# Kernel tuning notes

Measured on AMD Instinct MI355X. Metric: run time of the kernel, lower is better.

## Reference

```python
import jax, jax.numpy as jnp
import numpy as np

N, M = 30000, 16
NODE_F = 128          # node_fea_len
ORIG_F = 19           # 4 + location_num(15)
EDGE_F = 5
PI_IN = NODE_F + 10 + 5 + 5  # 148
BN_EPS = 1e-5


def _linear_init(k, fin, fout):
    s = 1.0 / np.sqrt(fin)
    kw, kb = jax.random.split(k)
    W = jax.random.uniform(kw, (fin, fout), jnp.float32, -s, s)
    b = jax.random.uniform(kb, (fout,), jnp.float32, -s, s)
    return W, b


def setup_inputs() -> dict:
    key = jax.random.key(0)
    ks = jax.random.split(key, 24)
    node_fea = jax.random.normal(ks[0], (N, ORIG_F), jnp.float32)
    edge_fea = jax.random.uniform(ks[1], (N, M, EDGE_F), dtype=jnp.float32)
    idx = jax.random.randint(ks[2], (N, M), 0, N)
    neg = jax.random.uniform(ks[3], (N, M)) < 0.1
    edge_fea_idx = jnp.where(neg, -1, idx)
    distance = jax.random.uniform(ks[4], (N, M), dtype=jnp.float32)

    emb_W, emb_b = _linear_init(ks[5], ORIG_F, NODE_F)
    fcW, fcB = [], []
    for i in range(3):
        W, b = _linear_init(ks[6 + i], 2 * NODE_F + EDGE_F, 2 * NODE_F)
        fcW.append(W); fcB.append(b)
    conv_fc_W = jnp.stack(fcW)   # [3, 261, 256]
    conv_fc_b = jnp.stack(fcB)   # [3, 256]
    bn1_g = jnp.ones((3, 2 * NODE_F), jnp.float32)
    bn1_b = jnp.zeros((3, 2 * NODE_F), jnp.float32)
    bn2_g = jnp.ones((3, NODE_F), jnp.float32)
    bn2_b = jnp.zeros((3, NODE_F), jnp.float32)

    def u(k, shape):  # MLP init: uniform(-0.08, 0.08)
        return jax.random.uniform(k, shape, jnp.float32, -0.08, 0.08)
    pi_W1 = u(ks[9], (PI_IN, 128)); pi_b1 = u(ks[10], (128,))
    pi_W2 = u(ks[11], (128, 256)); pi_b2 = u(ks[12], (256,))
    pi_W3 = u(ks[13], (256, 128)); pi_b3 = u(ks[14], (128,))
    pi_W4 = u(ks[15], (128, 1)); pi_b4 = u(ks[16], (1,))

    return dict(node_fea=node_fea, edge_fea=edge_fea, edge_fea_idx=edge_fea_idx,
                distance=distance, tp_type=1,
                emb_W=emb_W, emb_b=emb_b,
                conv_fc_W=conv_fc_W, conv_fc_b=conv_fc_b,
                bn1_g=bn1_g, bn1_b=bn1_b, bn2_g=bn2_g, bn2_b=bn2_b,
                pi_W1=pi_W1, pi_b1=pi_b1, pi_W2=pi_W2, pi_b2=pi_b2,
                pi_W3=pi_W3, pi_b3=pi_b3, pi_W4=pi_W4, pi_b4=pi_b4)


def _bn(x, g, b):  # BatchNorm1d in training mode: batch stats (biased var)
    mu = x.mean(0)
    var = x.var(0)
    return (x - mu) * jax.lax.rsqrt(var + BN_EPS) * g + b


def reference(node_fea, edge_fea, edge_fea_idx, distance, tp_type,
              emb_W, emb_b, conv_fc_W, conv_fc_b,
              bn1_g, bn1_b, bn2_g, bn2_b,
              pi_W1, pi_b1, pi_W2, pi_b2, pi_W3, pi_b3, pi_W4, pi_b4):
    n, m = edge_fea_idx.shape
    node = node_fea @ emb_W + emb_b                     # [N, 128]
    mask = (edge_fea_idx >= 0).astype(node.dtype)       # [N, M]

    for l in range(3):  # three CGCNN conv layers (structurally distinct params)
        nbr = node[edge_fea_idx]                        # gather, neg idx wraps like torch
        self_f = jnp.broadcast_to(node[:, None, :], (n, m, NODE_F))
        total = jnp.concatenate([self_f, nbr, edge_fea], axis=2)   # [N, M, 261]
        gated = total @ conv_fc_W[l] + conv_fc_b[l]                # [N, M, 256]
        gated = _bn(gated.reshape(-1, 2 * NODE_F), bn1_g[l], bn1_b[l]).reshape(n, m, 2 * NODE_F)
        filt, _ = jnp.split(gated, 2, axis=2)
        # NOTE: original code overwrites nbr_core with nbr_filter*mask (bug kept faithfully)
        filt = jax.nn.sigmoid(filt) * mask[..., None]
        core = filt * mask[..., None]
        summed = jnp.sum(filt * core, axis=1)                      # [N, 128]
        summed = _bn(summed, bn2_g[l], bn2_b[l])
        node = jax.nn.softplus(node + summed)

    # calculate_pi
    av = node[edge_fea_idx]                                        # [N, M, 128]
    tp_f = jnp.full((n, m, 5), float(tp_type), node.dtype)
    feat = jnp.concatenate([av,
                            jnp.tile(edge_fea, (1, 1, 2)),          # 10
                            jnp.repeat(distance[..., None], 5, 2),  # 5
                            tp_f], axis=2)                          # [N, M, 148]
    h = jax.nn.relu(feat @ pi_W1 + pi_b1)
    h = jax.nn.relu(h @ pi_W2 + pi_b2)
    h = jax.nn.relu(h @ pi_W3 + pi_b3)
    logits = h @ pi_W4 + pi_b4                                      # [N, M, 1]

    # get_action masked softmax: mask=1 where invalid
    amask = jnp.where((edge_fea_idx >= 0) & (edge_fea[:, :, 4] <= tp_type), 0.0, 1.0)
    logits_masked = logits - 1e8 * amask[..., None]
    prob = jax.nn.softmax(logits_masked.reshape(-1))                # [N*M]
    return prob
```

## Files before the change

### kernel.cpp

```cpp
#include <hip/hip_runtime.h>
#include <hip/hip_bf16.h>
#include <math.h>

#define NN 30000
#define MM 16
#define F 128
#define NMROWS (NN*MM)
constexpr float BN_EPS = 1e-5f;

using bf16x8 = __attribute__((ext_vector_type(8))) short;
using f32x4v = __attribute__((ext_vector_type(4))) float;

#define WS_NODE   0u
#define WS_S      3840000u
#define WS_T      7680000u
#define WS_SUM    11520000u
#define WS_LOGIT  15360000u
#define WS_RED    15840000u
#define WS_STATS  15841024u
#define ST_BN1SUM 0u
#define ST_BN1SQ  384u
#define ST_BN2SUM 768u
#define ST_BN2SQ  1152u
#define ST_W1E    2048u
#define ST_W1D    2688u
#define ST_B1EFF  2816u
#define ST_END    2944u

__device__ __forceinline__ float read_tp(const int* tp) {
  int ti = tp[0];
  return (ti >= -1000 && ti <= 1000) ? (float)ti : __int_as_float(ti);
}

__device__ __forceinline__ void split3(float x, short& a, short& b, short& c) {
  unsigned u0 = __float_as_uint(x);
  a = (short)(u0 >> 16);
  float r1 = x - __uint_as_float(u0 & 0xFFFF0000u);
  unsigned u1 = __float_as_uint(r1);
  b = (short)(u1 >> 16);
  float r2 = r1 - __uint_as_float(u1 & 0xFFFF0000u);
  c = (short)(__float_as_uint(r2) >> 16);
}

__global__ void k_pack_conv(const float* __restrict__ cW, const float* __restrict__ pW1,
                            short* __restrict__ convPack, short* __restrict__ wUp) {
  int tid = threadIdx.x, l = blockIdx.x;
  if (l < 3) {
    const float* Wl = cW + (size_t)l*261*256;
    short* dst = convPack + (size_t)l*98304;
    for (int it = 0; it < 8; ++it) {
      int slot = it*512 + tid;
      int ln = slot & 63, f = slot >> 6;
      int nt = f & 15, ks = f >> 4;
      int colg = nt*16 + (ln & 15);
      int kb = ks*32 + (ln >> 4)*8;
      bf16x8 h, m, lo;
      #pragma unroll
      for (int i = 0; i < 8; ++i) {
        int k = kb + i;
        float v = (colg < 128) ? Wl[(size_t)k*256 + colg]
                               : Wl[(size_t)(128 + k)*256 + (colg - 128)];
        short a, b, c; split3(v, a, b, c);
        h[i] = a; m[i] = b; lo[i] = c;
      }
      *(bf16x8*)&dst[((size_t)((0*4 + ks)*16 + nt))*512 + ln*8] = h;
      *(bf16x8*)&dst[((size_t)((1*4 + ks)*16 + nt))*512 + ln*8] = m;
      *(bf16x8*)&dst[((size_t)((2*4 + ks)*16 + nt))*512 + ln*8] = lo;
    }
  } else {
    for (int it = 0; it < 4; ++it) {
      int slot = it*512 + tid;
      int ln = slot & 63, f = slot >> 6;
      int nt = f & 7, ks = f >> 3;
      int colg = nt*16 + (ln & 15);
      int kb = ks*32 + (ln >> 4)*8;
      bf16x8 h, m, lo;
      #pragma unroll
      for (int i = 0; i < 8; ++i) {
        float v = pW1[(size_t)(kb + i)*128 + colg];
        short a, b, c; split3(v, a, b, c);
        h[i] = a; m[i] = b; lo[i] = c;
      }
      *(bf16x8*)&wUp[((size_t)((0*4 + ks)*8 + nt))*512 + ln*8] = h;
      *(bf16x8*)&wUp[((size_t)((1*4 + ks)*8 + nt))*512 + ln*8] = m;
      *(bf16x8*)&wUp[((size_t)((2*4 + ks)*8 + nt))*512 + ln*8] = lo;
    }
  }
}

__global__ __launch_bounds__(512, 2) void k_gemm(
    const float* __restrict__ nf, const float* __restrict__ embW, const float* __restrict__ embB,
    float* __restrict__ node, const float* __restrict__ summed,
    const float* __restrict__ bsum2, const float* __restrict__ bsq2,
    const float* __restrict__ g2, const float* __restrict__ b2,
    const short* __restrict__ Wp, const float* __restrict__ bias,
    float* __restrict__ outS, float* __restrict__ outT,
    int NT, int mode, int writeNode) {
  __shared__ __align__(16) short sb[64*392];
  __shared__ float nfL[64][20];
  __shared__ float ewL[19][128];
  int tid = threadIdx.x;
  int n0 = blockIdx.x*64;
  if (mode == 0) {
    for (int i = tid; i < 64*19; i += 512) {
      int r = i/19, k = i - r*19;
      int n = n0 + r;
      nfL[r][k] = (n < NN) ? nf[(size_t)n*19 + k] : 0.f;
    }
    for (int i = tid; i < 19*128; i += 512) ewL[i >> 7][i & 127] = embW[i];
  }
  __syncthreads();
  {
    int c = tid & 127, rg = tid >> 7;
    float scv = 0.f, shv = 0.f, eb = 0.f;
    if (mode == 0) {
      eb = embB[c];
    } else {
      const float inv_n = 1.f / (float)NN;
      float mu = bsum2[c]*inv_n;
      float var = bsq2[c]*inv_n - mu*mu;
      scv = g2[c]*rsqrtf(var + BN_EPS);
      shv = b2[c] - mu*scv;
    }
    #pragma unroll 4
    for (int rr = 0; rr < 16; ++rr) {
      int r = rg*16 + rr;
      int n = n0 + r;
      float v = 0.f;
      if (n < NN) {
        if (mode == 0) {
          v = eb;
          #pragma unroll
          for (int k = 0; k < 19; ++k) v = fmaf(nfL[r][k], ewL[k][c], v);
        } else {
          float x = node[(size_t)n*F + c] + fmaf(summed[(size_t)n*F + c], scv, shv);
          v = fmaxf(x, 0.f) + log1pf(expf(-fabsf(x)));
        }
        if (writeNode) node[(size_t)n*F + c] = v;
      }
      short s0, s1, s2; split3(v, s0, s1, s2);
      sb[r*392 + c] = s0; sb[r*392 + 128 + c] = s1; sb[r*392 + 256 + c] = s2;
    }
  }
  __syncthreads();
  int wv = tid >> 6, ln = tid & 63, lr = ln & 15, lg2 = ln >> 4;
  int ntpw = NT >> 3;
  f32x4v z4 = {0.f,0.f,0.f,0.f};
  f32x4v acc0[4] = {z4,z4,z4,z4};
  f32x4v acc1[4] = {z4,z4,z4,z4};
  int nt0 = wv*ntpw, nt1 = wv*ntpw + 1;
  for (int ks = 0; ks < 4; ++ks) {
    #pragma unroll
    for (int bs = 0; bs < 3; ++bs) {
      bf16x8 B0 = *(const bf16x8*)&Wp[((size_t)((bs*4 + ks)*NT + nt0))*512 + ln*8];
      bf16x8 B1 = B0;
      if (ntpw == 2) B1 = *(const bf16x8*)&Wp[((size_t)((bs*4 + ks)*NT + nt1))*512 + ln*8];
      int na = 3 - bs;
      #pragma unroll
      for (int as = 0; as < 3; ++as) {
        if (as >= na) break;
        #pragma unroll
        for (int mt = 0; mt < 4; ++mt) {
          bf16x8 a = *(const bf16x8*)&sb[(mt*16 + lr)*392 + as*128 + ks*32 + lg2*8];
          acc0[mt] = __builtin_amdgcn_mfma_f32_16x16x32_bf16(a, B0, acc0[mt], 0, 0, 0);
          if (ntpw == 2)
            acc1[mt] = __builtin_amdgcn_mfma_f32_16x16x32_bf16(a, B1, acc1[mt], 0, 0, 0);
        }
      }
    }
  }
  {
    int col = nt0*16 + lr;
    float bb = (col < 128) ? bias[col] : 0.f;
    #pragma unroll
    for (int mt = 0; mt < 4; ++mt) {
      #pragma unroll
      for (int rr = 0; rr < 4; ++rr) {
        int row = n0 + mt*16 + lg2*4 + rr;
        if (row < NN) {
          float x = acc0[mt][rr] + bb;
          if (col < 128) outS[(size_t)row*F + col] = x;
          else outT[(size_t)row*F + col - 128] = x;
        }
      }
    }
  }
  if (ntpw == 2) {
    int col = nt1*16 + lr;
    float bb = (col < 128) ? bias[col] : 0.f;
    #pragma unroll
    for (int mt = 0; mt < 4; ++mt) {
      #pragma unroll
      for (int rr = 0; rr < 4; ++rr) {
        int row = n0 + mt*16 + lg2*4 + rr;
        if (row < NN) {
          float x = acc1[mt][rr] + bb;
          if (col < 128) outS[(size_t)row*F + col] = x;
          else outT[(size_t)row*F + col - 128] = x;
        }
      }
    }
  }
}

__global__ __launch_bounds__(256, 8) void k_stats(
    const float* __restrict__ S, const float* __restrict__ T,
    const float* __restrict__ Wl, const float* __restrict__ edge,
    const int* __restrict__ idx,
    float* __restrict__ bsum, float* __restrict__ bsq) {
  __shared__ float eL[1280];
  __shared__ int gL[256];
  __shared__ float rA[256], rB[256];
  int tid = threadIdx.x;
  int n0 = blockIdx.x*16;
  for (int i = tid; i < 1280; i += 256) eL[i] = edge[(size_t)n0*80 + i];
  {
    int v = idx[n0*MM + tid];
    gL[tid] = v < 0 ? v + NN : v;
  }
  __syncthreads();
  int c = tid & 127, h = tid >> 7;
  float we[5];
  #pragma unroll
  for (int j = 0; j < 5; ++j) we[j] = Wl[(size_t)(256+j)*256 + c];
  float s1 = 0.f, s2 = 0.f;
  for (int nl = h*8; nl < h*8 + 8; ++nl) {
    float sv = S[(size_t)(n0+nl)*F + c];
    #pragma unroll
    for (int m = 0; m < MM; ++m) {
      int row = nl*MM + m;
      float g = sv + T[(size_t)gL[row]*F + c];
      const float* e = &eL[row*5];
      #pragma unroll
      for (int j = 0; j < 5; ++j) g = fmaf(e[j], we[j], g);
      s1 += g; s2 = fmaf(g, g, s2);
    }
  }
  rA[tid] = s1; rB[tid] = s2;
  __syncthreads();
  if (h == 0) {
    atomicAdd(&bsum[c], s1 + rA[128 + c]);
    atomicAdd(&bsq[c],  s2 + rB[128 + c]);
  }
}

__global__ __launch_bounds__(256, 6) void k_pass2(
    const float* __restrict__ S, const float* __restrict__ T,
    const float* __restrict__ Wl, const float* __restrict__ edge,
    const int* __restrict__ idx,
    const float* __restrict__ bsum1, const float* __restrict__ bsq1,
    const float* __restrict__ g1, const float* __restrict__ b1,
    float* __restrict__ summed, float* __restrict__ bsum2, float* __restrict__ bsq2) {
  __shared__ float eL[1280];
  __shared__ int gL[256];
  __shared__ float mk[256];
  __shared__ float rA[256], rB[256];
  int tid = threadIdx.x;
  int n0 = blockIdx.x*16;
  for (int i = tid; i < 1280; i += 256) eL[i] = edge[(size_t)n0*80 + i];
  {
    int v = idx[n0*MM + tid];
    mk[tid] = v >= 0 ? 1.f : 0.f;
    gL[tid] = v < 0 ? v + NN : v;
  }
  __syncthreads();
  int c = tid & 127, h = tid >> 7;
  float we[5];
  #pragma unroll
  for (int j = 0; j < 5; ++j) we[j] = Wl[(size_t)(256+j)*256 + c];
  float sc1v, sh1v;
  {
    const float inv_n = 1.f / (float)NMROWS;
    float mu = bsum1[c]*inv_n;
    float var = bsq1[c]*inv_n - mu*mu;
    sc1v = g1[c]*rsqrtf(var + BN_EPS);
    sh1v = b1[c] - mu*sc1v;
  }
  float st1 = 0.f, st2 = 0.f;
  for (int nl = h*8; nl < h*8 + 8; ++nl) {
    float sv = S[(size_t)(n0+nl)*F + c];
    float acc = 0.f;
    #pragma unroll
    for (int m = 0; m < MM; ++m) {
      int row = nl*MM + m;
      float g = sv + T[(size_t)gL[row]*F + c];
      const float* e = &eL[row*5];
      #pragma unroll
      for (int j = 0; j < 5; ++j) g = fmaf(e[j], we[j], g);
      float x = fmaf(g, sc1v, sh1v);
      float sig = 1.f/(1.f + expf(-x));
      acc = fmaf(mk[row]*sig, sig, acc);
    }
    summed[(size_t)(n0+nl)*F + c] = acc;
    st1 += acc; st2 = fmaf(acc, acc, st2);
  }
  rA[tid] = st1; rB[tid] = st2;
  __syncthreads();
  if (h == 0) {
    atomicAdd(&bsum2[c], st1 + rA[128 + c]);
    atomicAdd(&bsq2[c],  st2 + rB[128 + c]);
  }
}

__global__ void k_pi_const(const float* __restrict__ W1, const float* __restrict__ b1,
                           const int* __restrict__ tp,
                           float* __restrict__ w1e, float* __restrict__ w1d, float* __restrict__ b1eff) {
  int c = threadIdx.x;
  float t = read_tp(tp);
  #pragma unroll
  for (int j = 0; j < 5; ++j) w1e[j*128 + c] = W1[(128+j)*128 + c] + W1[(133+j)*128 + c];
  float d = 0.f;
  #pragma unroll
  for (int r = 138; r < 143; ++r) d += W1[r*128 + c];
  w1d[c] = d;
  float tt = 0.f;
  #pragma unroll
  for (int r = 143; r < 148; ++r) tt += W1[r*128 + c];
  b1eff[c] = b1[c] + t*tt;
}

__global__ void k_packw(const float* __restrict__ W2, const float* __restrict__ W3,
                        short* __restrict__ w2p, short* __restrict__ w3p) {
  int tid = threadIdx.x;
  if (blockIdx.x == 0) {
    for (int it = 0; it < 8; ++it) {
      int slot = it*512 + tid;
      int ln = slot & 63, fr = slot >> 6;
      int nt = fr & 15, ks = fr >> 4;
      int col = nt*16 + (ln & 15);
      int kb = ks*32 + (ln >> 4)*8;
      bf16x8 h, m, l;
      #pragma unroll
      for (int i = 0; i < 8; ++i) {
        short a, b, c;
        split3(W2[(size_t)(kb + i)*256 + col], a, b, c);
        h[i] = a; m[i] = b; l[i] = c;
      }
      *(bf16x8*)&w2p[((size_t)((0*4 + ks)*16 + nt))*512 + ln*8] = h;
      *(bf16x8*)&w2p[((size_t)((1*4 + ks)*16 + nt))*512 + ln*8] = m;
      *(bf16x8*)&w2p[((size_t)((2*4 + ks)*16 + nt))*512 + ln*8] = l;
    }
  } else {
    for (int it = 0; it < 8; ++it) {
      int slot = it*512 + tid;
      int ln = slot & 63, fr = slot >> 6;
      int nt = fr & 7, ks = fr >> 3;
      int col = nt*16 + (ln & 15);
      int kb = ks*32 + (ln >> 4)*8;
      bf16x8 h, m, l;
      #pragma unroll
      for (int i = 0; i < 8; ++i) {
        short a, b, c;
        split3(W3[(size_t)(kb + i)*128 + col], a, b, c);
        h[i] = a; m[i] = b; l[i] = c;
      }
      *(bf16x8*)&w3p[((size_t)((0*8 + ks)*8 + nt))*512 + ln*8] = h;
      *(bf16x8*)&w3p[((size_t)((1*8 + ks)*8 + nt))*512 + ln*8] = m;
      *(bf16x8*)&w3p[((size_t)((2*8 + ks)*8 + nt))*512 + ln*8] = l;
    }
  }
}

__global__ __launch_bounds__(512, 6) void k_pi_mfma(
    const float* __restrict__ U, const float* __restrict__ b2,
    const float* __restrict__ b3, const float* __restrict__ W4, const float* __restrict__ b4,
    const short* __restrict__ w2p, const short* __restrict__ w3p,
    const float* __restrict__ edge, const int* __restrict__ idx, const float* __restrict__ dist,
    const int* __restrict__ tp,
    const float* __restrict__ w1e, const float* __restrict__ w1d,
    float* __restrict__ lgt) {
  __shared__ __align__(16) short buf[32*776];
  __shared__ float eeL[32][5];
  __shared__ float ddL[32];
  __shared__ int gxL[32], ivL[32];
  __shared__ float part[8][32];
  int tid = threadIdx.x;
  int rb = blockIdx.x*32;
  for (int i = tid; i < 160; i += 512) eeL[i/5][i%5] = edge[(size_t)rb*5 + i];
  if (tid < 32) {
    int v = idx[rb + tid];
    ivL[tid] = v;
    gxL[tid] = v < 0 ? v + NN : v;
    ddL[tid] = dist[rb + tid];
  }
  __syncthreads();

  {
    int c = tid & 127, rg = tid >> 7;
    float wd = w1d[c];
    float wE[5];
    #pragma unroll
    for (int j = 0; j < 5; ++j) wE[j] = w1e[j*128 + c];
    #pragma unroll
    for (int rr = 0; rr < 8; ++rr) {
      int r = rg*8 + rr;
      float v = U[(size_t)gxL[r]*F + c];
      v = fmaf(ddL[r], wd, v);
      #pragma unroll
      for (int j = 0; j < 5; ++j) v = fmaf(eeL[r][j], wE[j], v);
      v = fmaxf(v, 0.f);
      short s0, s1, s2; split3(v, s0, s1, s2);
      buf[r*392 + c] = s0; buf[r*392 + 128 + c] = s1; buf[r*392 + 256 + c] = s2;
    }
  }
  __syncthreads();

  int wv = tid >> 6, ln = tid & 63;
  int lr = ln & 15, lg2 = ln >> 4;
  f32x4v zz = {0.f, 0.f, 0.f, 0.f};

  f32x4v accB[2][2];
  accB[0][0] = zz; accB[0][1] = zz; accB[1][0] = zz; accB[1][1] = zz;
  {
    int nt0 = wv*2, nt1 = wv*2 + 1;
    for (int ks = 0; ks < 4; ++ks) {
      #pragma unroll
      for (int bs = 0; bs < 3; ++bs) {
        bf16x8 B0 = *(const bf16x8*)&w2p[((size_t)((bs*4 + ks)*16 + nt0))*512 + ln*8];
        bf16x8 B1 = *(const bf16x8*)&w2p[((size_t)((bs*4 + ks)*16 + nt1))*512 + ln*8];
        int na = 3 - bs;
        #pragma unroll
        for (int as = 0; as < 3; ++as) {
          if (as >= na) break;
          #pragma unroll
          for (int mt = 0; mt < 2; ++mt) {
            bf16x8 a = *(const bf16x8*)&buf[(mt*16 + lr)*392 + as*128 + ks*32 + lg2*8];
            accB[mt][0] = __builtin_amdgcn_mfma_f32_16x16x32_bf16(a, B0, accB[mt][0], 0, 0, 0);
            accB[mt][1] = __builtin_amdgcn_mfma_f32_16x16x32_bf16(a, B1, accB[mt][1], 0, 0, 0);
          }
        }
      }
    }
  }
  __syncthreads();
  {
    #pragma unroll
    for (int ntl = 0; ntl < 2; ++ntl) {
      int col = (wv*2 + ntl)*16 + lr;
      float bb = b2[col];
      #pragma unroll
      for (int mt = 0; mt < 2; ++mt) {
        #pragma unroll
        for (int r = 0; r < 4; ++r) {
          int row = mt*16 + lg2*4 + r;
          float x = fmaxf(accB[mt][ntl][r] + bb, 0.f);
          short s0, s1, s2; split3(x, s0, s1, s2);
          buf[row*776 + col] = s0; buf[row*776 + 256 + col] = s1; buf[row*776 + 512 + col] = s2;
        }
      }
    }
  }
  __syncthreads();

  f32x4v accC[2];
  accC[0] = zz; accC[1] = zz;
  {
    for (int ks = 0; ks < 8; ++ks) {
      #pragma unroll
      for (int bs = 0; bs < 3; ++bs) {
        bf16x8 B = *(const bf16x8*)&w3p[((size_t)((bs*8 + ks)*8 + wv))*512 + ln*8];
        int na = 3 - bs;
        #pragma unroll
        for (int as = 0; as < 3; ++as) {
          if (as >= na) break;
          #pragma unroll
          for (int mt = 0; mt < 2; ++mt) {
            bf16x8 a = *(const bf16x8*)&buf[(mt*16 + lr)*776 + as*256 + ks*32 + lg2*8];
            accC[mt] = __builtin_amdgcn_mfma_f32_16x16x32_bf16(a, B, accC[mt], 0, 0, 0);
          }
        }
      }
    }
  }

  {
    float w4c = W4[wv*16 + lr];
    float b3c = b3[wv*16 + lr];
    #pragma unroll
    for (int mt = 0; mt < 2; ++mt) {
      float p0 = fmaxf(accC[mt][0] + b3c, 0.f) * w4c;
      float p1 = fmaxf(accC[mt][1] + b3c, 0.f) * w4c;
      float p2 = fmaxf(accC[mt][2] + b3c, 0.f) * w4c;
      float p3 = fmaxf(accC[mt][3] + b3c, 0.f) * w4c;
      #pragma unroll
      for (int off = 1; off < 16; off <<= 1) {
        p0 += __shfl_xor(p0, off, 16);
        p1 += __shfl_xor(p1, off, 16);
        p2 += __shfl_xor(p2, off, 16);
        p3 += __shfl_xor(p3, off, 16);
      }
      if (lr == 0) {
        int row = mt*16 + lg2*4;
        part[wv][row]   = p0;
        part[wv][row+1] = p1;
        part[wv][row+2] = p2;
        part[wv][row+3] = p3;
      }
    }
  }
  __syncthreads();
  if (tid < 32) {
    float s = 0.f;
    #pragma unroll
    for (int w = 0; w < 8; ++w) s += part[w][tid];
    float tpf = read_tp(tp);
    float lgv = s + b4[0];
    float am = (ivL[tid] >= 0 && eeL[tid][4] <= tpf) ? 0.f : 1.f;
    lgt[rb + tid] = lgv - 1e8f*am;
  }
}

__global__ void k_pass1(const float* __restrict__ lg, float* __restrict__ red) {
  __shared__ float r[256];
  int t = threadIdx.x;
  float m = -3.4e38f;
  for (int i = blockIdx.x*256 + t; i < NMROWS; i += 512*256) m = fmaxf(m, lg[i]);
  r[t] = m; __syncthreads();
  for (int s = 128; s > 0; s >>= 1) {
    if (t < s) r[t] = fmaxf(r[t], r[t + s]);
    __syncthreads();
  }
  float bm = r[0];
  __syncthreads();
  float sum = 0.f;
  for (int i = blockIdx.x*256 + t; i < NMROWS; i += 512*256) sum += expf(lg[i] - bm);
  r[t] = sum; __syncthreads();
  for (int s = 128; s > 0; s >>= 1) {
    if (t < s) r[t] += r[t + s];
    __syncthreads();
  }
  if (t == 0) { red[blockIdx.x] = bm; red[512 + blockIdx.x] = r[0]; }
}

__global__ void k_out2(const float* __restrict__ lg, const float* __restrict__ red,
                       float* __restrict__ out) {
  __shared__ float r[256], z[256];
  int t = threadIdx.x;
  float m = fmaxf(red[t], red[t + 256]);
  r[t] = m; __syncthreads();
  for (int s = 128; s > 0; s >>= 1) {
    if (t < s) r[t] = fmaxf(r[t], r[t + s]);
    __syncthreads();
  }
  float gmax = r[0];
  __syncthreads();
  float zz = red[512 + t]*expf(red[t] - gmax) + red[768 + t]*expf(red[256 + t] - gmax);
  z[t] = zz; __syncthreads();
  for (int s = 128; s > 0; s >>= 1) {
    if (t < s) z[t] += z[t + s];
    __syncthreads();
  }
  float invZ = 1.f / z[0];
  int i = blockIdx.x*256 + t;
  if (i < NMROWS) out[i] = expf(lg[i] - gmax)*invZ;
}

extern "C" void kernel_launch(void* const* d_in, const int* in_sizes, int n_in,
                              void* d_out, int out_size, void* d_ws, size_t ws_size,
                              hipStream_t stream) {
  (void)in_sizes; (void)n_in; (void)out_size;
  const float* node_fea = (const float*)d_in[0];
  const float* edge_fea = (const float*)d_in[1];
  const int*   eidx     = (const int*)d_in[2];
  const float* dist     = (const float*)d_in[3];
  const int*   tp       = (const int*)d_in[4];
  const float* emb_W    = (const float*)d_in[5];
  const float* emb_b    = (const float*)d_in[6];
  const float* cW       = (const float*)d_in[7];
  const float* cb       = (const float*)d_in[8];
  const float* bn1g     = (const float*)d_in[9];
  const float* bn1b     = (const float*)d_in[10];
  const float* bn2g     = (const float*)d_in[11];
  const float* bn2b     = (const float*)d_in[12];
  const float* pW1      = (const float*)d_in[13];
  const float* pb1      = (const float*)d_in[14];
  const float* pW2      = (const float*)d_in[15];
  const float* pb2      = (const float*)d_in[16];
  const float* pW3      = (const float*)d_in[17];
  const float* pb3      = (const float*)d_in[18];
  const float* pW4      = (const float*)d_in[19];
  const float* pb4      = (const float*)d_in[20];
  float* out = (float*)d_out;
  float* ws  = (float*)d_ws;

  if (ws_size < (size_t)(WS_STATS + ST_END)*sizeof(float)) return;

  float* stats = ws + WS_STATS;
  float* node   = ws + WS_NODE;
  float* Sbuf   = ws + WS_S;
  float* Tbuf   = ws + WS_T;
  float* sumbuf = ws + WS_SUM;
  hipMemsetAsync(stats, 0, 1536*sizeof(float), stream);

  short* convPack = (short*)(ws + WS_LOGIT);
  short* wUp      = (short*)(ws + WS_LOGIT + 300000u);
  k_pack_conv<<<4, 512, 0, stream>>>(cW, pW1, convPack, wUp);
  k_pi_const<<<1, 128, 0, stream>>>(pW1, pb1, tp, stats + ST_W1E, stats + ST_W1D, stats + ST_B1EFF);

  for (int l = 0; l < 3; ++l) {
    const float* Wl = cW + (size_t)l*261*256;
    if (l == 0) {
      k_gemm<<<469, 512, 0, stream>>>(node_fea, emb_W, emb_b, node,
                                      nullptr, nullptr, nullptr, nullptr, nullptr,
                                      convPack, cb, Sbuf, Tbuf, 16, 0, 1);
    } else {
      k_gemm<<<469, 512, 0, stream>>>(nullptr, nullptr, nullptr, node,
                                      sumbuf, stats + ST_BN2SUM + (l-1)*128, stats + ST_BN2SQ + (l-1)*128,
                                      bn2g + (l-1)*128, bn2b + (l-1)*128,
                                      convPack + (size_t)l*98304, cb + l*256, Sbuf, Tbuf, 16, 1, 1);
    }
    k_stats<<<1875, 256, 0, stream>>>(Sbuf, Tbuf, Wl, edge_fea, eidx,
                                      stats + ST_BN1SUM + l*128, stats + ST_BN1SQ + l*128);
    k_pass2<<<1875, 256, 0, stream>>>(Sbuf, Tbuf, Wl, edge_fea, eidx,
                                      stats + ST_BN1SUM + l*128, stats + ST_BN1SQ + l*128,
                                      bn1g + l*256, bn1b + l*256,
                                      sumbuf, stats + ST_BN2SUM + l*128, stats + ST_BN2SQ + l*128);
  }

  short* w2p = (short*)(ws + WS_T);
  short* w3p = (short*)(ws + WS_T + 49152u);
  k_packw<<<2, 512, 0, stream>>>(pW2, pW3, w2p, w3p);

  k_gemm<<<469, 512, 0, stream>>>(nullptr, nullptr, nullptr, node,
                                  sumbuf, stats + ST_BN2SUM + 2*128, stats + ST_BN2SQ + 2*128,
                                  bn2g + 2*128, bn2b + 2*128,
                                  wUp, stats + ST_B1EFF, Sbuf, Sbuf, 8, 1, 0);

  k_pi_mfma<<<15000, 512, 0, stream>>>(Sbuf, pb2, pb3, pW4, pb4, w2p, w3p,
                                       edge_fea, eidx, dist, tp,
                                       stats + ST_W1E, stats + ST_W1D, ws + WS_LOGIT);

  k_pass1<<<512, 256, 0, stream>>>(ws + WS_LOGIT, ws + WS_RED);
  k_out2<<<1875, 256, 0, stream>>>(ws + WS_LOGIT, ws + WS_RED, out);
}
```

Baseline: 1.170 ms.

## Use 32x32x16 MFMA in pi MLP with split-K; halve k_gemm row tile

The pi-MLP kernel now uses 32x32x16 bf16 MFMA instructions instead of 16x16x32. The weight packing is rearranged to the 32-wide fragment layout. Layer 3 is split across wave pairs along K, and the partial sums are combined through shared memory before the W4 dot-product reduction. Separately, k_gemm processes 32 rows per block instead of 64, with twice as many blocks and a higher occupancy hint, to spread the work across more CUs. The trade-offs are extra LDS traffic and syncs for the split-K combine, and a longer shuffle reduction over 16 registers.

```diff
diff --git a/kernel.cpp b/kernel.cpp
--- a/kernel.cpp
+++ b/kernel.cpp
@@ -10,6 +10,7 @@
 
 using bf16x8 = __attribute__((ext_vector_type(8))) short;
 using f32x4v = __attribute__((ext_vector_type(4))) float;
+using f32x16v = __attribute__((ext_vector_type(16))) float;
 
 #define WS_NODE   0u
 #define WS_S      3840000u
@@ -88,7 +89,7 @@
   }
 }
 
-__global__ __launch_bounds__(512, 2) void k_gemm(
+__global__ __launch_bounds__(512, 6) void k_gemm(
     const float* __restrict__ nf, const float* __restrict__ embW, const float* __restrict__ embB,
     float* __restrict__ node, const float* __restrict__ summed,
     const float* __restrict__ bsum2, const float* __restrict__ bsq2,
@@ -96,13 +97,13 @@
     const short* __restrict__ Wp, const float* __restrict__ bias,
     float* __restrict__ outS, float* __restrict__ outT,
     int NT, int mode, int writeNode) {
-  __shared__ __align__(16) short sb[64*392];
-  __shared__ float nfL[64][20];
+  __shared__ __align__(16) short sb[32*392];
+  __shared__ float nfL[32][20];
   __shared__ float ewL[19][128];
   int tid = threadIdx.x;
-  int n0 = blockIdx.x*64;
+  int n0 = blockIdx.x*32;
   if (mode == 0) {
-    for (int i = tid; i < 64*19; i += 512) {
+    for (int i = tid; i < 32*19; i += 512) {
       int r = i/19, k = i - r*19;
       int n = n0 + r;
       nfL[r][k] = (n < NN) ? nf[(size_t)n*19 + k] : 0.f;
@@ -122,9 +123,9 @@
       scv = g2[c]*rsqrtf(var + BN_EPS);
       shv = b2[c] - mu*scv;
     }
-    #pragma unroll 4
-    for (int rr = 0; rr < 16; ++rr) {
-      int r = rg*16 + rr;
+    #pragma unroll
+    for (int rr = 0; rr < 8; ++rr) {
+      int r = rg*8 + rr;
       int n = n0 + r;
       float v = 0.f;
       if (n < NN) {
@@ -146,8 +147,8 @@
   int wv = tid >> 6, ln = tid & 63, lr = ln & 15, lg2 = ln >> 4;
   int ntpw = NT >> 3;
   f32x4v z4 = {0.f,0.f,0.f,0.f};
-  f32x4v acc0[4] = {z4,z4,z4,z4};
-  f32x4v acc1[4] = {z4,z4,z4,z4};
+  f32x4v acc0[2] = {z4,z4};
+  f32x4v acc1[2] = {z4,z4};
   int nt0 = wv*ntpw, nt1 = wv*ntpw + 1;
   for (int ks = 0; ks < 4; ++ks) {
     #pragma unroll
@@ -160,7 +161,7 @@
       for (int as = 0; as < 3; ++as) {
         if (as >= na) break;
         #pragma unroll
-        for (int mt = 0; mt < 4; ++mt) {
+        for (int mt = 0; mt < 2; ++mt) {
           bf16x8 a = *(const bf16x8*)&sb[(mt*16 + lr)*392 + as*128 + ks*32 + lg2*8];
           acc0[mt] = __builtin_amdgcn_mfma_f32_16x16x32_bf16(a, B0, acc0[mt], 0, 0, 0);
           if (ntpw == 2)
@@ -173,7 +174,7 @@
     int col = nt0*16 + lr;
     float bb = (col < 128) ? bias[col] : 0.f;
     #pragma unroll
-    for (int mt = 0; mt < 4; ++mt) {
+    for (int mt = 0; mt < 2; ++mt) {
       #pragma unroll
       for (int rr = 0; rr < 4; ++rr) {
         int row = n0 + mt*16 + lg2*4 + rr;
@@ -189,7 +190,7 @@
     int col = nt1*16 + lr;
     float bb = (col < 128) ? bias[col] : 0.f;
     #pragma unroll
-    for (int mt = 0; mt < 4; ++mt) {
+    for (int mt = 0; mt < 2; ++mt) {
       #pragma unroll
       for (int rr = 0; rr < 4; ++rr) {
         int row = n0 + mt*16 + lg2*4 + rr;
@@ -326,9 +327,9 @@
     for (int it = 0; it < 8; ++it) {
       int slot = it*512 + tid;
       int ln = slot & 63, fr = slot >> 6;
-      int nt = fr & 15, ks = fr >> 4;
-      int col = nt*16 + (ln & 15);
-      int kb = ks*32 + (ln >> 4)*8;
+      int nt = fr & 7, ks = fr >> 3;
+      int col = nt*32 + (ln & 31);
+      int kb = ks*16 + (ln >> 5)*8;
       bf16x8 h, m, l;
       #pragma unroll
       for (int i = 0; i < 8; ++i) {
@@ -336,17 +337,17 @@
         split3(W2[(size_t)(kb + i)*256 + col], a, b, c);
         h[i] = a; m[i] = b; l[i] = c;
       }
-      *(bf16x8*)&w2p[((size_t)((0*4 + ks)*16 + nt))*512 + ln*8] = h;
-      *(bf16x8*)&w2p[((size_t)((1*4 + ks)*16 + nt))*512 + ln*8] = m;
-      *(bf16x8*)&w2p[((size_t)((2*4 + ks)*16 + nt))*512 + ln*8] = l;
+      *(bf16x8*)&w2p[((size_t)((0*8 + ks)*8 + nt))*512 + ln*8] = h;
+      *(bf16x8*)&w2p[((size_t)((1*8 + ks)*8 + nt))*512 + ln*8] = m;
+      *(bf16x8*)&w2p[((size_t)((2*8 + ks)*8 + nt))*512 + ln*8] = l;
     }
   } else {
     for (int it = 0; it < 8; ++it) {
       int slot = it*512 + tid;
       int ln = slot & 63, fr = slot >> 6;
-      int nt = fr & 7, ks = fr >> 3;
-      int col = nt*16 + (ln & 15);
-      int kb = ks*32 + (ln >> 4)*8;
+      int nt = fr & 3, ks = fr >> 2;
+      int col = nt*32 + (ln & 31);
+      int kb = ks*16 + (ln >> 5)*8;
       bf16x8 h, m, l;
       #pragma unroll
       for (int i = 0; i < 8; ++i) {
@@ -354,9 +355,9 @@
         split3(W3[(size_t)(kb + i)*128 + col], a, b, c);
         h[i] = a; m[i] = b; l[i] = c;
       }
-      *(bf16x8*)&w3p[((size_t)((0*8 + ks)*8 + nt))*512 + ln*8] = h;
-      *(bf16x8*)&w3p[((size_t)((1*8 + ks)*8 + nt))*512 + ln*8] = m;
-      *(bf16x8*)&w3p[((size_t)((2*8 + ks)*8 + nt))*512 + ln*8] = l;
+      *(bf16x8*)&w3p[((size_t)((0*16 + ks)*4 + nt))*512 + ln*8] = h;
+      *(bf16x8*)&w3p[((size_t)((1*16 + ks)*4 + nt))*512 + ln*8] = m;
+      *(bf16x8*)&w3p[((size_t)((2*16 + ks)*4 + nt))*512 + ln*8] = l;
     }
   }
 }
@@ -373,7 +374,7 @@
   __shared__ float eeL[32][5];
   __shared__ float ddL[32];
   __shared__ int gxL[32], ivL[32];
-  __shared__ float part[8][32];
+  __shared__ float part[4][32];
   int tid = threadIdx.x;
   int rb = blockIdx.x*32;
   for (int i = tid; i < 160; i += 512) eeL[i/5][i%5] = edge[(size_t)rb*5 + i];
@@ -406,103 +407,88 @@
   __syncthreads();
 
   int wv = tid >> 6, ln = tid & 63;
-  int lr = ln & 15, lg2 = ln >> 4;
-  f32x4v zz = {0.f, 0.f, 0.f, 0.f};
-
-  f32x4v accB[2][2];
-  accB[0][0] = zz; accB[0][1] = zz; accB[1][0] = zz; accB[1][1] = zz;
+  int lc = ln & 31, l5 = ln >> 5;
+  f32x16v zz16 = {0.f,0.f,0.f,0.f,0.f,0.f,0.f,0.f,0.f,0.f,0.f,0.f,0.f,0.f,0.f,0.f};
+
+  f32x16v accB = zz16;
+  for (int ks = 0; ks < 8; ++ks) {
+    #pragma unroll
+    for (int bs = 0; bs < 3; ++bs) {
+      bf16x8 B = *(const bf16x8*)&w2p[((size_t)((bs*8 + ks)*8 + wv))*512 + ln*8];
+      int na = 3 - bs;
+      #pragma unroll
+      for (int as = 0; as < 3; ++as) {
+        if (as >= na) break;
+        bf16x8 a = *(const bf16x8*)&buf[lc*392 + as*128 + ks*16 + l5*8];
+        accB = __builtin_amdgcn_mfma_f32_32x32x16_bf16(a, B, accB, 0, 0, 0);
+      }
+    }
+  }
+  __syncthreads();
   {
-    int nt0 = wv*2, nt1 = wv*2 + 1;
-    for (int ks = 0; ks < 4; ++ks) {
-      #pragma unroll
-      for (int bs = 0; bs < 3; ++bs) {
-        bf16x8 B0 = *(const bf16x8*)&w2p[((size_t)((bs*4 + ks)*16 + nt0))*512 + ln*8];
-        bf16x8 B1 = *(const bf16x8*)&w2p[((size_t)((bs*4 + ks)*16 + nt1))*512 + ln*8];
-        int na = 3 - bs;
-        #pragma unroll
-        for (int as = 0; as < 3; ++as) {
-          if (as >= na) break;
-          #pragma unroll
-          for (int mt = 0; mt < 2; ++mt) {
-            bf16x8 a = *(const bf16x8*)&buf[(mt*16 + lr)*392 + as*128 + ks*32 + lg2*8];
-            accB[mt][0] = __builtin_amdgcn_mfma_f32_16x16x32_bf16(a, B0, accB[mt][0], 0, 0, 0);
-            accB[mt][1] = __builtin_amdgcn_mfma_f32_16x16x32_bf16(a, B1, accB[mt][1], 0, 0, 0);
-          }
-        }
-      }
-    }
-  }
-  __syncthreads();
-  {
-    #pragma unroll
-    for (int ntl = 0; ntl < 2; ++ntl) {
-      int col = (wv*2 + ntl)*16 + lr;
-      float bb = b2[col];
-      #pragma unroll
-      for (int mt = 0; mt < 2; ++mt) {
-        #pragma unroll
-        for (int r = 0; r < 4; ++r) {
-          int row = mt*16 + lg2*4 + r;
-          float x = fmaxf(accB[mt][ntl][r] + bb, 0.f);
-          short s0, s1, s2; split3(x, s0, s1, s2);
-          buf[row*776 + col] = s0; buf[row*776 + 256 + col] = s1; buf[row*776 + 512 + col] = s2;
-        }
-      }
-    }
-  }
-  __syncthreads();
-
-  f32x4v accC[2];
-  accC[0] = zz; accC[1] = zz;
-  {
-    for (int ks = 0; ks < 8; ++ks) {
-      #pragma unroll
-      for (int bs = 0; bs < 3; ++bs) {
-        bf16x8 B = *(const bf16x8*)&w3p[((size_t)((bs*8 + ks)*8 + wv))*512 + ln*8];
-        int na = 3 - bs;
-        #pragma unroll
-        for (int as = 0; as < 3; ++as) {
-          if (as >= na) break;
-          #pragma unroll
-          for (int mt = 0; mt < 2; ++mt) {
-            bf16x8 a = *(const bf16x8*)&buf[(mt*16 + lr)*776 + as*256 + ks*32 + lg2*8];
-            accC[mt] = __builtin_amdgcn_mfma_f32_16x16x32_bf16(a, B, accC[mt], 0, 0, 0);
-          }
-        }
-      }
-    }
-  }
-
-  {
-    float w4c = W4[wv*16 + lr];
-    float b3c = b3[wv*16 + lr];
-    #pragma unroll
-    for (int mt = 0; mt < 2; ++mt) {
-      float p0 = fmaxf(accC[mt][0] + b3c, 0.f) * w4c;
-      float p1 = fmaxf(accC[mt][1] + b3c, 0.f) * w4c;
-      float p2 = fmaxf(accC[mt][2] + b3c, 0.f) * w4c;
-      float p3 = fmaxf(accC[mt][3] + b3c, 0.f) * w4c;
-      #pragma unroll
-      for (int off = 1; off < 16; off <<= 1) {
-        p0 += __shfl_xor(p0, off, 16);
-        p1 += __shfl_xor(p1, off, 16);
-        p2 += __shfl_xor(p2, off, 16);
-        p3 += __shfl_xor(p3, off, 16);
-      }
-      if (lr == 0) {
-        int row = mt*16 + lg2*4;
-        part[wv][row]   = p0;
-        part[wv][row+1] = p1;
-        part[wv][row+2] = p2;
-        part[wv][row+3] = p3;
+    int col = wv*32 + lc;
+    float bb = b2[col];
+    #pragma unroll
+    for (int reg = 0; reg < 16; ++reg) {
+      int row = (reg & 3) + 8*(reg >> 2) + 4*l5;
+      float x = fmaxf(accB[reg] + bb, 0.f);
+      short s0, s1, s2; split3(x, s0, s1, s2);
+      buf[row*776 + col] = s0; buf[row*776 + 256 + col] = s1; buf[row*776 + 512 + col] = s2;
+    }
+  }
+  __syncthreads();
+
+  f32x16v accC = zz16;
+  int ntc = wv >> 1, kh = wv & 1;
+  for (int ks = 0; ks < 8; ++ks) {
+    int kstep = kh*8 + ks;
+    #pragma unroll
+    for (int bs = 0; bs < 3; ++bs) {
+      bf16x8 B = *(const bf16x8*)&w3p[((size_t)((bs*16 + kstep)*4 + ntc))*512 + ln*8];
+      int na = 3 - bs;
+      #pragma unroll
+      for (int as = 0; as < 3; ++as) {
+        if (as >= na) break;
+        bf16x8 a = *(const bf16x8*)&buf[lc*776 + as*256 + kstep*16 + l5*8];
+        accC = __builtin_amdgcn_mfma_f32_32x32x16_bf16(a, B, accC, 0, 0, 0);
+      }
+    }
+  }
+  __syncthreads();
+  float* scr = (float*)buf;
+  if (kh == 1) {
+    int base = (ntc*64 + ln)*17;
+    #pragma unroll
+    for (int reg = 0; reg < 16; ++reg) scr[base + reg] = accC[reg];
+  }
+  __syncthreads();
+
+  if (kh == 0) {
+    int base = (ntc*64 + ln)*17;
+    float w4c = W4[ntc*32 + lc];
+    float b3c = b3[ntc*32 + lc];
+    float p[16];
+    #pragma unroll
+    for (int reg = 0; reg < 16; ++reg) {
+      float v = accC[reg] + scr[base + reg];
+      p[reg] = fmaxf(v + b3c, 0.f) * w4c;
+    }
+    #pragma unroll
+    for (int off = 1; off < 32; off <<= 1) {
+      #pragma unroll
+      for (int reg = 0; reg < 16; ++reg) p[reg] += __shfl_xor(p[reg], off);
+    }
+    if (lc == 0) {
+      #pragma unroll
+      for (int reg = 0; reg < 16; ++reg) {
+        int row = (reg & 3) + 8*(reg >> 2) + 4*l5;
+        part[ntc][row] = p[reg];
       }
     }
   }
   __syncthreads();
   if (tid < 32) {
-    float s = 0.f;
-    #pragma unroll
-    for (int w = 0; w < 8; ++w) s += part[w][tid];
+    float s = part[0][tid] + part[1][tid] + part[2][tid] + part[3][tid];
     float tpf = read_tp(tp);
     float lgv = s + b4[0];
     float am = (ivL[tid] >= 0 && eeL[tid][4] <= tpf) ? 0.f : 1.f;
@@ -600,11 +586,11 @@
   for (int l = 0; l < 3; ++l) {
     const float* Wl = cW + (size_t)l*261*256;
     if (l == 0) {
-      k_gemm<<<469, 512, 0, stream>>>(node_fea, emb_W, emb_b, node,
+      k_gemm<<<938, 512, 0, stream>>>(node_fea, emb_W, emb_b, node,
                                       nullptr, nullptr, nullptr, nullptr, nullptr,
                                       convPack, cb, Sbuf, Tbuf, 16, 0, 1);
     } else {
-      k_gemm<<<469, 512, 0, stream>>>(nullptr, nullptr, nullptr, node,
+      k_gemm<<<938, 512, 0, stream>>>(nullptr, nullptr, nullptr, node,
                                       sumbuf, stats + ST_BN2SUM + (l-1)*128, stats + ST_BN2SQ + (l-1)*128,
                                       bn2g + (l-1)*128, bn2b + (l-1)*128,
                                       convPack + (size_t)l*98304, cb + l*256, Sbuf, Tbuf, 16, 1, 1);
@@ -621,7 +607,7 @@
   short* w3p = (short*)(ws + WS_T + 49152u);
   k_packw<<<2, 512, 0, stream>>>(pW2, pW3, w2p, w3p);
 
-  k_gemm<<<469, 512, 0, stream>>>(nullptr, nullptr, nullptr, node,
+  k_gemm<<<938, 512, 0, stream>>>(nullptr, nullptr, nullptr, node,
                                   sumbuf, stats + ST_BN2SUM + 2*128, stats + ST_BN2SQ + 2*128,
                                   bn2g + 2*128, bn2b + 2*128,
                                   wUp, stats + ST_B1EFF, Sbuf, Sbuf, 8, 1, 0);
```

Result: no change. 1.154 ms (-1.3%).
